# Kernel tuning notes

Measured on AMD Instinct MI355X. Metric: run time of the kernel, lower is better.

## Reference

```python
import jax, jax.numpy as jnp
import numpy as np

E = 8        # num discriminators == num adapters (layer_structure = [1]*8)
D = 1024     # feature_dim
DO = 1024    # out_feature_dim
R = 64       # adapter bottleneck rank
H = 256      # discriminator hidden dim
B, T = 8, 2048


def setup_inputs() -> dict:
    key = jax.random.key(0)
    ks = jax.random.split(key, 12)
    s = lambda k, shape, fan: jax.random.normal(k, shape, jnp.float32) / np.sqrt(fan)
    return {
        "x": jax.random.normal(ks[0], (B, T, D), jnp.float32),
        # base layer (Linear D -> DO)
        "W_base": s(ks[1], (D, DO), D),
        "b_base": jnp.zeros((DO,), jnp.float32),
        # stacked discriminator autoencoders: D -> H -> D
        "Wd1": s(ks[2], (E, D, H), D),
        "bd1": jnp.zeros((E, H), jnp.float32),
        "Wd2": s(ks[3], (E, H, D), H),
        "bd2": jnp.zeros((E, D), jnp.float32),
        # stacked bottleneck adapters: D -> R -> DO
        "Wa_down": s(ks[4], (E, D, R), D),
        "ba_down": jnp.zeros((E, R), jnp.float32),
        "Wa_up": s(ks[5], (E, R, DO), R),
        "ba_up": jnp.zeros((E, DO), jnp.float32),
    }


def reference(x, W_base, b_base, Wd1, bd1, Wd2, bd2, Wa_down, ba_down, Wa_up, ba_up):
    # base path
    base = jnp.einsum("btd,do->bto", x, W_base) + b_base

    # all discriminators in parallel (stack_module_state + vmap equivalent)
    h = jax.nn.relu(jnp.einsum("btd,edh->ebth", x, Wd1) + bd1[:, None, None, :])
    recon = jnp.einsum("ebth,ehd->ebtd", h, Wd2) + bd2[:, None, None, :]
    # per-(discriminator, sample) reconstruction loss -> [E, B]
    losses = jnp.mean((recon - x[None]) ** 2, axis=(2, 3))

    # top-1 routing: argmin over discriminators per sample; identity mapping to adapters
    idx = jnp.argmin(losses, axis=0)  # [B]

    # grouped adapter forward: gather per-sample weights, batched GEMM
    a = jax.nn.relu(jnp.einsum("btd,bdr->btr", x, Wa_down[idx]) + ba_down[idx][:, None, :])
    adapter_out = jnp.einsum("btr,bro->bto", a, Wa_up[idx]) + ba_up[idx][:, None, :]

    return base + adapter_out
```

## Files before the change

kernel.cpp:

```cpp
#include <hip/hip_runtime.h>

typedef __bf16 bf16x8 __attribute__((ext_vector_type(8)));
typedef float f32x4 __attribute__((ext_vector_type(4)));
typedef unsigned short ushort_t;

#define THREADS 256
#define PTHREADS 512

__device__ __forceinline__ unsigned short f2bf(float f) {
  unsigned int u = __builtin_bit_cast(unsigned int, f);
  u += 0x7fffu + ((u >> 16) & 1u);
  return (unsigned short)(u >> 16);
}

__device__ __forceinline__ float bf2f(ushort_t u) {
  unsigned int v = ((unsigned int)u) << 16;
  return __builtin_bit_cast(float, v);
}

__device__ __forceinline__ void gload_lds16(const ushort_t* g, ushort_t* l) {
  __builtin_amdgcn_global_load_lds(
      (const __attribute__((address_space(1))) void*)g,
      (__attribute__((address_space(3))) void*)l, 16, 0, 0);
}

template <int N>
__device__ __forceinline__ void wait_vmcnt() {
  if constexpr (N == 0)
    asm volatile("s_waitcnt vmcnt(0)" ::: "memory");
  else if constexpr (N == 3)
    asm volatile("s_waitcnt vmcnt(3)" ::: "memory");
  else if constexpr (N == 6)
    asm volatile("s_waitcnt vmcnt(6)" ::: "memory");
}

__device__ __forceinline__ void block_barrier() {
  asm volatile("" ::: "memory");
  __builtin_amdgcn_s_barrier();
  asm volatile("" ::: "memory");
}

__global__ void cast_x_kernel(const float4* __restrict__ src,
                              ushort4* __restrict__ dst, int n4) {
  int stride = gridDim.x * blockDim.x;
  for (int i = blockIdx.x * blockDim.x + threadIdx.x; i < n4; i += stride) {
    float4 v = src[i];
    ushort4 o;
    o.x = f2bf(v.x); o.y = f2bf(v.y); o.z = f2bf(v.z); o.w = f2bf(v.w);
    dst[i] = o;
  }
}

__global__ void transpose_all_kernel(
    const float* __restrict__ Wd1, const float* __restrict__ Wd2,
    const float* __restrict__ Wb, const float* __restrict__ Wad,
    const float* __restrict__ Wau, ushort_t* __restrict__ Wd1T,
    ushort_t* __restrict__ Wd2T, ushort_t* __restrict__ WbT,
    ushort_t* __restrict__ WadT, ushort_t* __restrict__ WauT,
    float* __restrict__ losses) {
  __shared__ float t[32][33];
  int b = blockIdx.x;
  int tx = threadIdx.x, ty = threadIdx.y;
  int ft = ty * 32 + tx;
  if (b == 0 && ft < 64) losses[ft] = 0.f;

  const float* src;
  ushort_t* dst;
  int R, C, z, cx, ry;
  if (b < 2048) {
    src = Wd1; dst = Wd1T; R = 1024; C = 256;
    z = b >> 8; int rem = b & 255; cx = rem & 7; ry = rem >> 3;
  } else if (b < 4096) {
    int bb = b - 2048;
    src = Wd2; dst = Wd2T; R = 256; C = 1024;
    z = bb >> 8; int rem = bb & 255; cx = rem & 31; ry = rem >> 5;
  } else if (b < 5120) {
    int bb = b - 4096;
    src = Wb; dst = WbT; R = 1024; C = 1024;
    z = 0; cx = bb & 31; ry = bb >> 5;
  } else if (b < 5632) {
    int bb = b - 5120;
    src = Wad; dst = WadT; R = 1024; C = 64;
    z = bb >> 6; int rem = bb & 63; cx = rem & 1; ry = rem >> 1;
  } else {
    int bb = b - 5632;
    src = Wau; dst = WauT; R = 64; C = 1024;
    z = bb >> 6; int rem = bb & 63; cx = rem & 31; ry = rem >> 5;
  }
  size_t zoff = (size_t)z * R * C;
  src += zoff; dst += zoff;
  int c0 = cx * 32, r0 = ry * 32;
#pragma unroll
  for (int i = 0; i < 4; ++i)
    t[ty + 8 * i][tx] = src[(size_t)(r0 + ty + 8 * i) * C + c0 + tx];
  __syncthreads();
#pragma unroll
  for (int i = 0; i < 4; ++i)
    dst[(size_t)(c0 + ty + 8 * i) * R + r0 + tx] = f2bf(t[tx][ty + 8 * i]);
}

#define ACC_ZERO(acc, MM, NN)                        \
  _Pragma("unroll") for (int _i = 0; _i < MM; ++_i)  \
  _Pragma("unroll") for (int _j = 0; _j < NN; ++_j)  \
      acc[_i][_j] = (f32x4){0.f, 0.f, 0.f, 0.f};

#define ACC_INIT(acc)  \
  f32x4 acc[4][4];     \
  ACC_ZERO(acc, 4, 4)

__device__ __forceinline__ int sw(int row) { return (row >> 1) & 3; }

__device__ __forceinline__ bf16x8 frag_sw(const ushort_t* lds, int row, int q) {
  int slot = q ^ sw(row);
  return *(const bf16x8*)(lds + (row * 4 + slot) * 8);
}

template <int BM, int BN>
__device__ __forceinline__ void stage_p(const ushort_t* __restrict__ A,
                                        size_t lda, int arow0,
                                        const ushort_t* __restrict__ BT,
                                        size_t ldb, int brow0, int k0,
                                        ushort_t* As, ushort_t* Bs, int tid) {
#pragma unroll
  for (int i = 0; i < BM * 4 / PTHREADS; ++i) {
    int c = tid + i * PTHREADS;
    int row = c >> 2, slot = c & 3;
    int g = slot ^ sw(row);
    gload_lds16(A + (size_t)(arow0 + row) * lda + k0 + g * 8, As + c * 8);
  }
#pragma unroll
  for (int i = 0; i < BN * 4 / PTHREADS; ++i) {
    int c = tid + i * PTHREADS;
    int row = c >> 2, slot = c & 3;
    int g = slot ^ sw(row);
    gload_lds16(BT + (size_t)(brow0 + row) * ldb + k0 + g * 8, Bs + c * 8);
  }
}

template <int BM, int BN>
__device__ __forceinline__ void pipe_kloop(const ushort_t* __restrict__ A,
                                           size_t lda, int arow0,
                                           const ushort_t* __restrict__ BT,
                                           size_t ldb, int brow0, int K,
                                           ushort_t* smem, int tid, int wm,
                                           int wn, f32x4 acc[4][4]) {
  constexpr int ASLOT = BM * 32, BSLOT = BN * 32;
  ushort_t* Asl = smem;
  ushort_t* Bsl = smem + 3 * ASLOT;
  int lane = tid & 63;
  int r = lane & 15, q = lane >> 4;
  int nt = K >> 5;
  stage_p<BM, BN>(A, lda, arow0, BT, ldb, brow0, 0, Asl, Bsl, tid);
  if (nt > 1)
    stage_p<BM, BN>(A, lda, arow0, BT, ldb, brow0, 32, Asl + ASLOT,
                    Bsl + BSLOT, tid);
  for (int t = 0; t < nt; ++t) {
    if (t + 1 < nt)
      wait_vmcnt<3>();
    else
      wait_vmcnt<0>();
    block_barrier();
    if (t + 2 < nt) {
      int s = (t + 2) % 3;
      stage_p<BM, BN>(A, lda, arow0, BT, ldb, brow0, (t + 2) * 32,
                      Asl + s * ASLOT, Bsl + s * BSLOT, tid);
    }
    int cur = t % 3;
    const ushort_t* Ac = Asl + cur * ASLOT;
    const ushort_t* Bc = Bsl + cur * BSLOT;
    bf16x8 af[4], bg[4];
#pragma unroll
    for (int mi = 0; mi < 4; ++mi)
      af[mi] = frag_sw(Ac, wm * 64 + mi * 16 + r, q);
#pragma unroll
    for (int ni = 0; ni < 4; ++ni)
      bg[ni] = frag_sw(Bc, wn * 64 + ni * 16 + r, q);
    __builtin_amdgcn_s_setprio(1);
#pragma unroll
    for (int mi = 0; mi < 4; ++mi)
#pragma unroll
      for (int ni = 0; ni < 4; ++ni)
        acc[mi][ni] = __builtin_amdgcn_mfma_f32_16x16x32_bf16(
            af[mi], bg[ni], acc[mi][ni], 0, 0, 0);
    __builtin_amdgcn_s_setprio(0);
  }
  block_barrier();
}

#define PIPE_LDS_BYTES ((3 * (256 * 32) + 3 * (128 * 32)) * 2)

__global__ __launch_bounds__(PTHREADS, 4) void disc_h_kernel(
    const ushort_t* __restrict__ x_bf, const ushort_t* __restrict__ Wd1T,
    const float* __restrict__ bd1, ushort_t* __restrict__ h) {
  extern __shared__ ushort_t smem[];
  int b = blockIdx.x;
  int work = (b & 7) * 128 + (b >> 3);
  int m0 = (work >> 4) * 256;
  int n0 = (work & 15) * 128;
  int tid = threadIdx.x, wid = tid >> 6, lane = tid & 63;
  int wm = wid >> 1, wn = wid & 1;
  ACC_INIT(acc);
  pipe_kloop<256, 128>(x_bf, 1024, m0, Wd1T, 1024, n0, 1024, smem, tid, wm,
                       wn, acc);
  int r = lane & 15, q = lane >> 4;
#pragma unroll
  for (int ni = 0; ni < 4; ++ni) {
    int col = n0 + wn * 64 + ni * 16 + r;
    float bias = bd1[col];
    int e = col >> 8, nn = col & 255;
    ushort_t* hp = h + (size_t)e * 16384 * 256 + nn;
#pragma unroll
    for (int mi = 0; mi < 4; ++mi) {
      int rowb = m0 + wm * 64 + mi * 16 + q * 4;
#pragma unroll
      for (int j = 0; j < 4; ++j) {
        float v = fmaxf(acc[mi][ni][j] + bias, 0.f);
        hp[(size_t)(rowb + j) * 256] = f2bf(v);
      }
    }
  }
}

__global__ __launch_bounds__(PTHREADS, 4) void disc_loss_kernel(
    const ushort_t* __restrict__ h, const ushort_t* __restrict__ Wd2T,
    const float* __restrict__ bd2, const ushort_t* __restrict__ x_bf,
    float* __restrict__ losses) {
  extern __shared__ ushort_t smem[];
  __shared__ float red[8];
  int b = blockIdx.x;
  int work = (b & 7) * 512 + (b >> 3);
  int e = work >> 9;
  int m0 = ((work >> 3) & 63) * 256;
  int n0 = (work & 7) * 128;
  int tid = threadIdx.x, wid = tid >> 6, lane = tid & 63;
  int wm = wid >> 1, wn = wid & 1;
  int r = lane & 15, q = lane >> 4;
  const ushort_t* hA = h + (size_t)e * 16384 * 256;
  const ushort_t* W2 = Wd2T + (size_t)e * 1024 * 256;

  ACC_INIT(acc);
  pipe_kloop<256, 128>(hA, 256, m0, W2, 256, n0, 256, smem, tid, wm, wn, acc);

  float s = 0.f;
#pragma unroll
  for (int ni = 0; ni < 4; ++ni) {
    int colg = n0 + wn * 64 + ni * 16 + r;
    float bias = bd2[e * 1024 + colg];
#pragma unroll
    for (int mi = 0; mi < 4; ++mi) {
      int rowg = m0 + wm * 64 + mi * 16 + q * 4;
#pragma unroll
      for (int j = 0; j < 4; ++j) {
        float v = acc[mi][ni][j] + bias -
                  bf2f(x_bf[(size_t)(rowg + j) * 1024 + colg]);
        s += v * v;
      }
    }
  }
#pragma unroll
  for (int off = 32; off > 0; off >>= 1) s += __shfl_down(s, off);
  if (lane == 0) red[wid] = s;
  __syncthreads();
  if (tid == 0) {
    float t = 0.f;
#pragma unroll
    for (int i = 0; i < 8; ++i) t += red[i];
    atomicAdd(&losses[e * 8 + (m0 >> 11)], t);
  }
}

__global__ void argmin_kernel(const float* __restrict__ losses,
                              int* __restrict__ idx) {
  int b = threadIdx.x;
  if (b < 8) {
    float best = losses[b];
    int bi = 0;
    for (int e = 1; e < 8; ++e) {
      float v = losses[e * 8 + b];
      if (v < best) { best = v; bi = e; }
    }
    idx[b] = bi;
  }
}

__global__ __launch_bounds__(PTHREADS, 4) void final_kernel(
    const ushort_t* __restrict__ x, const ushort_t* __restrict__ WbT,
    const float* __restrict__ b_base, const ushort_t* __restrict__ a,
    const ushort_t* __restrict__ WauT, const float* __restrict__ ba_up,
    const int* __restrict__ idx, float* __restrict__ out) {
  extern __shared__ ushort_t smem[];
  int b = blockIdx.x;
  int work = (b & 7) * 64 + (b >> 3);
  int m0 = (work >> 3) * 256;
  int n0 = (work & 7) * 128;
  int e = idx[m0 >> 11];
  int tid = threadIdx.x, wid = tid >> 6, lane = tid & 63;
  int wm = wid >> 1, wn = wid & 1;
  ACC_INIT(acc);
  pipe_kloop<256, 128>(x, 1024, m0, WbT, 1024, n0, 1024, smem, tid, wm, wn,
                       acc);
  pipe_kloop<256, 128>(a, 64, m0, WauT + (size_t)e * 1024 * 64, 64, n0, 64,
                       smem, tid, wm, wn, acc);
  int r = lane & 15, q = lane >> 4;
#pragma unroll
  for (int ni = 0; ni < 4; ++ni) {
    int col = n0 + wn * 64 + ni * 16 + r;
    float bias = b_base[col] + ba_up[e * 1024 + col];
#pragma unroll
    for (int mi = 0; mi < 4; ++mi) {
      int rowb = m0 + wm * 64 + mi * 16 + q * 4;
#pragma unroll
      for (int j = 0; j < 4; ++j)
        out[(size_t)(rowb + j) * 1024 + col] = acc[mi][ni][j] + bias;
    }
  }
}

template <int BM, int BN>
__device__ __forceinline__ void stage_tiles(const ushort_t* __restrict__ A,
                                            size_t lda, int arow0,
                                            const ushort_t* __restrict__ BT,
                                            size_t ldb, int brow0, int k0,
                                            ushort_t* As, ushort_t* Bs,
                                            int tid) {
#pragma unroll
  for (int i = 0; i < BM / 64; ++i) {
    int c = tid + i * THREADS;
    int row = c >> 2, slot = c & 3;
    int g = slot ^ sw(row);
    gload_lds16(A + (size_t)(arow0 + row) * lda + k0 + g * 8, As + c * 8);
  }
#pragma unroll
  for (int i = 0; i < BN / 64; ++i) {
    int c = tid + i * THREADS;
    int row = c >> 2, slot = c & 3;
    int g = slot ^ sw(row);
    gload_lds16(BT + (size_t)(brow0 + row) * ldb + k0 + g * 8, Bs + c * 8);
  }
}

__global__ __launch_bounds__(THREADS) void adapter_down_kernel(
    const ushort_t* __restrict__ x, const ushort_t* __restrict__ WadT,
    const float* __restrict__ ba_down, const int* __restrict__ idx,
    ushort_t* __restrict__ a) {
  __shared__ ushort_t As[64 * 32], Bs[64 * 32];
  int m0 = blockIdx.x * 64;
  int e = idx[m0 >> 11];
  int tid = threadIdx.x, wid = tid >> 6, lane = tid & 63;
  int r = lane & 15, q = lane >> 4;
  const ushort_t* W = WadT + (size_t)e * 64 * 1024;
  f32x4 acc[4];
#pragma unroll
  for (int ni = 0; ni < 4; ++ni) acc[ni] = (f32x4){0.f, 0.f, 0.f, 0.f};
  for (int k0 = 0; k0 < 1024; k0 += 32) {
    stage_tiles<64, 64>(x, 1024, m0, W, 1024, 0, k0, As, Bs, tid);
    __syncthreads();
    bf16x8 af = frag_sw(As, wid * 16 + r, q);
#pragma unroll
    for (int ni = 0; ni < 4; ++ni) {
      bf16x8 bg = frag_sw(Bs, ni * 16 + r, q);
      acc[ni] = __builtin_amdgcn_mfma_f32_16x16x32_bf16(af, bg, acc[ni], 0, 0, 0);
    }
    __syncthreads();
  }
#pragma unroll
  for (int ni = 0; ni < 4; ++ni) {
    int col = ni * 16 + r;
    float bias = ba_down[e * 64 + col];
    int rowb = m0 + wid * 16 + q * 4;
#pragma unroll
    for (int j = 0; j < 4; ++j) {
      float v = fmaxf(acc[ni][j] + bias, 0.f);
      a[(size_t)(rowb + j) * 64 + col] = f2bf(v);
    }
  }
}

extern "C" void kernel_launch(void* const* d_in, const int* in_sizes, int n_in,
                              void* d_out, int out_size, void* d_ws,
                              size_t ws_size, hipStream_t stream) {
  const float* x       = (const float*)d_in[0];
  const float* W_base  = (const float*)d_in[1];
  const float* b_base  = (const float*)d_in[2];
  const float* Wd1     = (const float*)d_in[3];
  const float* bd1     = (const float*)d_in[4];
  const float* Wd2     = (const float*)d_in[5];
  const float* bd2     = (const float*)d_in[6];
  const float* Wa_down = (const float*)d_in[7];
  const float* ba_down = (const float*)d_in[8];
  const float* Wa_up   = (const float*)d_in[9];
  const float* ba_up   = (const float*)d_in[10];
  float* out = (float*)d_out;

  char* w = (char*)d_ws;
  size_t off = 0;
  auto alloc = [&](size_t bytes) {
    void* p = w + off;
    off += (bytes + 255) & ~(size_t)255;
    return p;
  };
  ushort_t* x_bf = (ushort_t*)alloc((size_t)16384 * 1024 * 2);
  ushort_t* Wd1T = (ushort_t*)alloc((size_t)8 * 256 * 1024 * 2);
  ushort_t* Wd2T = (ushort_t*)alloc((size_t)8 * 1024 * 256 * 2);
  ushort_t* WbT  = (ushort_t*)alloc((size_t)1024 * 1024 * 2);
  ushort_t* WadT = (ushort_t*)alloc((size_t)8 * 64 * 1024 * 2);
  ushort_t* WauT = (ushort_t*)alloc((size_t)8 * 1024 * 64 * 2);
  ushort_t* abuf = (ushort_t*)alloc((size_t)16384 * 64 * 2);
  float* losses  = (float*)alloc(64 * 4);
  int* idxb      = (int*)alloc(64);
  size_t hbytes = (size_t)8 * 16384 * 256 * 2;
  ushort_t* h = (ws_size >= off + hbytes) ? (ushort_t*)alloc(hbytes)
                                          : (ushort_t*)d_out;

  (void)hipFuncSetAttribute((const void*)disc_h_kernel,
                            hipFuncAttributeMaxDynamicSharedMemorySize,
                            PIPE_LDS_BYTES);
  (void)hipFuncSetAttribute((const void*)disc_loss_kernel,
                            hipFuncAttributeMaxDynamicSharedMemorySize,
                            PIPE_LDS_BYTES);
  (void)hipFuncSetAttribute((const void*)final_kernel,
                            hipFuncAttributeMaxDynamicSharedMemorySize,
                            PIPE_LDS_BYTES);

  cast_x_kernel<<<2048, 256, 0, stream>>>((const float4*)x, (ushort4*)x_bf,
                                          16777216 / 4);
  transpose_all_kernel<<<6144, dim3(32, 8), 0, stream>>>(
      Wd1, Wd2, W_base, Wa_down, Wa_up, Wd1T, Wd2T, WbT, WadT, WauT, losses);

  disc_h_kernel<<<1024, PTHREADS, PIPE_LDS_BYTES, stream>>>(x_bf, Wd1T, bd1, h);
  disc_loss_kernel<<<4096, PTHREADS, PIPE_LDS_BYTES, stream>>>(h, Wd2T, bd2,
                                                               x_bf, losses);
  argmin_kernel<<<1, 64, 0, stream>>>(losses, idxb);

  adapter_down_kernel<<<256, THREADS, 0, stream>>>(x_bf, WadT, ba_down, idxb,
                                                   abuf);
  final_kernel<<<512, PTHREADS, PIPE_LDS_BYTES, stream>>>(x_bf, WbT, b_base,
                                                          abuf, WauT, ba_up,
                                                          idxb, out);
}
```

Before: 273.2 us.

## Make disc_loss persistent over eight M-tiles with continuous cross-tile pipeline

The disc_loss kernel drops from 4096 blocks to 512. Each block now processes eight consecutive 256-row tiles for a fixed expert and N slice, and runs one continuous 3-slot LDS pipeline across all 64 k-steps instead of refilling the pipeline for every tile. The loss epilogue runs every 8 steps and accumulates into a per-thread scalar, so there is one atomicAdd per block. This removes per-tile prologue and drain costs and reduces atomic traffic, but 512 blocks may underfill the GPU compared with 4096, and the loss epilogue now sits inside the main loop.

```diff
diff --git a/kernel.cpp b/kernel.cpp
--- a/kernel.cpp
+++ b/kernel.cpp
@@ -227,45 +227,92 @@
     float* __restrict__ losses) {
   extern __shared__ ushort_t smem[];
   __shared__ float red[8];
+  constexpr int ASLOT = 256 * 32, BSLOT = 128 * 32;
+  ushort_t* Asl = smem;
+  ushort_t* Bsl = smem + 3 * ASLOT;
+
   int b = blockIdx.x;
-  int work = (b & 7) * 512 + (b >> 3);
-  int e = work >> 9;
-  int m0 = ((work >> 3) & 63) * 256;
-  int n0 = (work & 7) * 128;
+  int e = b & 7;
+  int idx = b >> 3;
+  int n0 = (idx & 7) * 128;
+  int mg = idx >> 3;
   int tid = threadIdx.x, wid = tid >> 6, lane = tid & 63;
   int wm = wid >> 1, wn = wid & 1;
   int r = lane & 15, q = lane >> 4;
   const ushort_t* hA = h + (size_t)e * 16384 * 256;
   const ushort_t* W2 = Wd2T + (size_t)e * 1024 * 256;
 
+  float bias[4];
+#pragma unroll
+  for (int ni = 0; ni < 4; ++ni)
+    bias[ni] = bd2[e * 1024 + n0 + wn * 64 + ni * 16 + r];
+
+  auto stage_s = [&](int s, int slot) {
+    int u = s >> 3, k0 = (s & 7) * 32;
+    int m0 = (mg * 8 + u) * 256;
+    stage_p<256, 128>(hA, 256, m0, W2, 256, n0, k0, Asl + slot * ASLOT,
+                      Bsl + slot * BSLOT, tid);
+  };
+
+  float loss = 0.f;
   ACC_INIT(acc);
-  pipe_kloop<256, 128>(hA, 256, m0, W2, 256, n0, 256, smem, tid, wm, wn, acc);
-
-  float s = 0.f;
-#pragma unroll
-  for (int ni = 0; ni < 4; ++ni) {
-    int colg = n0 + wn * 64 + ni * 16 + r;
-    float bias = bd2[e * 1024 + colg];
-#pragma unroll
-    for (int mi = 0; mi < 4; ++mi) {
-      int rowg = m0 + wm * 64 + mi * 16 + q * 4;
-#pragma unroll
-      for (int j = 0; j < 4; ++j) {
-        float v = acc[mi][ni][j] + bias -
-                  bf2f(x_bf[(size_t)(rowg + j) * 1024 + colg]);
-        s += v * v;
+
+  stage_s(0, 0);
+  stage_s(1, 1);
+  for (int s = 0; s < 64; ++s) {
+    if (s == 63)
+      wait_vmcnt<0>();
+    else
+      wait_vmcnt<3>();
+    block_barrier();
+    if (s + 2 < 64) stage_s(s + 2, (s + 2) % 3);
+    int cur = s % 3;
+    const ushort_t* Ac = Asl + cur * ASLOT;
+    const ushort_t* Bc = Bsl + cur * BSLOT;
+    bf16x8 af[4], bg[4];
+#pragma unroll
+    for (int mi = 0; mi < 4; ++mi)
+      af[mi] = frag_sw(Ac, wm * 64 + mi * 16 + r, q);
+#pragma unroll
+    for (int ni = 0; ni < 4; ++ni)
+      bg[ni] = frag_sw(Bc, wn * 64 + ni * 16 + r, q);
+    __builtin_amdgcn_s_setprio(1);
+#pragma unroll
+    for (int mi = 0; mi < 4; ++mi)
+#pragma unroll
+      for (int ni = 0; ni < 4; ++ni)
+        acc[mi][ni] = __builtin_amdgcn_mfma_f32_16x16x32_bf16(
+            af[mi], bg[ni], acc[mi][ni], 0, 0, 0);
+    __builtin_amdgcn_s_setprio(0);
+    if ((s & 7) == 7) {
+      int m0 = (mg * 8 + (s >> 3)) * 256;
+#pragma unroll
+      for (int ni = 0; ni < 4; ++ni) {
+        int colg = n0 + wn * 64 + ni * 16 + r;
+#pragma unroll
+        for (int mi = 0; mi < 4; ++mi) {
+          int rowg = m0 + wm * 64 + mi * 16 + q * 4;
+#pragma unroll
+          for (int j = 0; j < 4; ++j) {
+            float v = acc[mi][ni][j] + bias[ni] -
+                      bf2f(x_bf[(size_t)(rowg + j) * 1024 + colg]);
+            loss += v * v;
+          }
+        }
       }
-    }
-  }
-#pragma unroll
-  for (int off = 32; off > 0; off >>= 1) s += __shfl_down(s, off);
-  if (lane == 0) red[wid] = s;
+      ACC_ZERO(acc, 4, 4);
+    }
+  }
+
+#pragma unroll
+  for (int off = 32; off > 0; off >>= 1) loss += __shfl_down(loss, off);
+  if (lane == 0) red[wid] = loss;
   __syncthreads();
   if (tid == 0) {
     float t = 0.f;
 #pragma unroll
     for (int i = 0; i < 8; ++i) t += red[i];
-    atomicAdd(&losses[e * 8 + (m0 >> 11)], t);
+    atomicAdd(&losses[e * 8 + mg], t);
   }
 }
 
@@ -428,8 +475,8 @@
       Wd1, Wd2, W_base, Wa_down, Wa_up, Wd1T, Wd2T, WbT, WadT, WauT, losses);
 
   disc_h_kernel<<<1024, PTHREADS, PIPE_LDS_BYTES, stream>>>(x_bf, Wd1T, bd1, h);
-  disc_loss_kernel<<<4096, PTHREADS, PIPE_LDS_BYTES, stream>>>(h, Wd2T, bd2,
-                                                               x_bf, losses);
+  disc_loss_kernel<<<512, PTHREADS, PIPE_LDS_BYTES, stream>>>(h, Wd2T, bd2,
+                                                              x_bf, losses);
   argmin_kernel<<<1, 64, 0, stream>>>(losses, idxb);
 
   adapter_down_kernel<<<256, THREADS, 0, stream>>>(x_bf, WadT, ba_down, idxb,
```

Measured after the change: 324.6 us. 18.8% more time.
